# Optimization experiments

Measured on AMD Instinct MI355X. Metric: run time of the kernel, lower is better.

Reference implementation:

```python
import jax, jax.numpy as jnp
import numpy as np

T, N, E, F_IN, H1, H2, NUM_GRAPHS, K = 8, 10000, 320000, 32, 32, 16, 64, 5


def setup_inputs() -> dict:
    key = jax.random.key(0)
    ks = jax.random.split(key, 16)
    p = lambda k, shape: jax.random.normal(k, shape, jnp.float32) * 0.05
    return {
        "x": jax.random.normal(ks[0], (T, N, F_IN), jnp.float32),
        "edge_index": jax.random.randint(ks[1], (2, E), 0, N),
        "edge_attr": jax.random.uniform(ks[2], (E,), jnp.float32),
        "batch": jnp.sort(jax.random.randint(ks[3], (N,), 0, NUM_GRAPHS)),
        "Wx1": p(ks[4], (4, K, F_IN, H1)),
        "bx1": jnp.zeros((4, H1), jnp.float32),
        "Wh1": p(ks[5], (4, K, H1, H1)),
        "bh1": jnp.zeros((4, H1), jnp.float32),
        "wc1": p(ks[6], (3, H1)),
        "b1": jnp.zeros((4, H1), jnp.float32),
        "Wx2": p(ks[7], (4, K, H1, H2)),
        "bx2": jnp.zeros((4, H2), jnp.float32),
        "Wh2": p(ks[8], (4, K, H2, H2)),
        "bh2": jnp.zeros((4, H2), jnp.float32),
        "wc2": p(ks[9], (3, H2)),
        "b2": jnp.zeros((4, H2), jnp.float32),
        "lin_w": p(ks[10], (H2, 1)),
        "lin_b": jnp.zeros((1,), jnp.float32),
    }


def _forward(x, edge_index, edge_attr, batch,
             Wx1, bx1, Wh1, bh1, wc1, b1,
             Wx2, bx2, Wh2, bh2, wc2, b2, lin_w, lin_b):
    src, dst = edge_index[0], edge_index[1]
    n = x.shape[1]

    # ChebConv sym normalization with lambda_max=2: L_hat = L_sym - I = -D^{-1/2} A D^{-1/2}
    deg = jax.ops.segment_sum(edge_attr, src, num_segments=n)
    deg_safe = jnp.where(deg > 0, deg, 1.0)
    dis = jnp.where(deg > 0, jax.lax.rsqrt(deg_safe), 0.0)
    wnorm = dis[src] * edge_attr * dis[dst]  # [E]

    def Lhat(z):  # z: [N, C] -> L_hat @ z
        return -jax.ops.segment_sum(wnorm[:, None] * z[src], dst, num_segments=n)

    def cheb(z, W, b):  # W: [K, C_in, C_out], b: [C_out]
        out = z @ W[0]
        Tp, Tc = z, Lhat(z)  # T_0, T_1
        out = out + Tc @ W[1]
        for k in range(2, W.shape[0]):
            Tp, Tc = Tc, 2.0 * Lhat(Tc) - Tp
            out = out + Tc @ W[k]
        return out + b

    def cell(X, H, C, Wx, bx, Wh, bh, wc, bg):
        # gate order: 0=i, 1=f, 2=c, 3=o (GConvLSTM with peepholes)
        I = jax.nn.sigmoid(cheb(X, Wx[0], bx[0]) + cheb(H, Wh[0], bh[0]) + wc[0] * C + bg[0])
        Fg = jax.nn.sigmoid(cheb(X, Wx[1], bx[1]) + cheb(H, Wh[1], bh[1]) + wc[1] * C + bg[1])
        Ct = jnp.tanh(cheb(X, Wx[2], bx[2]) + cheb(H, Wh[2], bh[2]) + bg[2])
        Cn = Fg * C + I * Ct
        O = jax.nn.sigmoid(cheb(X, Wx[3], bx[3]) + cheb(H, Wh[3], bh[3]) + wc[2] * Cn + bg[3])
        return O * jnp.tanh(Cn), Cn

    @jax.checkpoint
    def step(carry, xt):
        h1, c1, h2, c2 = carry
        h1, c1 = cell(xt, h1, c1, Wx1, bx1, Wh1, bh1, wc1, b1)
        h2, c2 = cell(h1, h2, c2, Wx2, bx2, Wh2, bh2, wc2, b2)
        return (h1, c1, h2, c2), None

    z32 = jnp.zeros((n, Wh1.shape[-1]), x.dtype)
    z16 = jnp.zeros((n, Wh2.shape[-1]), x.dtype)
    (h1, c1, h2, c2), _ = jax.lax.scan(step, (z32, z32, z16, z16), x)

    # relu/dropout on h2 in the torch code is dead code (its result is unused in eval)
    u = jax.ops.segment_sum(h2, batch, num_segments=NUM_GRAPHS)  # global_add_pool
    return (u @ lin_w + lin_b).reshape(-1)


def reference(x, edge_index, edge_attr, batch,
              Wx1, bx1, Wh1, bh1, wc1, b1,
              Wx2, bx2, Wh2, bh2, wc2, b2, lin_w, lin_b):
    return _forward(x, edge_index, edge_attr, batch,
                    Wx1, bx1, Wh1, bh1, wc1, b1,
                    Wx2, bx2, Wh2, bh2, wc2, b2, lin_w, lin_b)
```

## Files before the change

### kernel.cpp

```cpp
#include <hip/hip_runtime.h>
#include <hip/hip_bf16.h>

#define TT 8
#define NN 10000
#define EE 320000
#define NG 64
#define SZS 400
#define SZH 384

typedef short v8s __attribute__((ext_vector_type(8)));
typedef _Float16 v8h __attribute__((ext_vector_type(8)));
typedef float v4f __attribute__((ext_vector_type(4)));

__device__ __forceinline__ float sigmf(float x){ return 1.f/(1.f+expf(-x)); }
__device__ __forceinline__ unsigned short f2h(float f){ _Float16 h=(_Float16)f; return __builtin_bit_cast(unsigned short,h); }
__device__ __forceinline__ float h2f(unsigned short s){ return (float)__builtin_bit_cast(_Float16,s); }
__device__ __forceinline__ unsigned pack2h(float x,float y){ return (unsigned)f2h(x) | ((unsigned)f2h(y)<<16); }
__device__ __forceinline__ size_t fragidx(int TK,int row,int c){
  int tile=row>>4, m=row&15, kt=c>>5, cc=c&31;
  return ((size_t)(tile*TK+kt)*64 + (cc>>3)*16 + m)*8 + (cc&7);
}

__global__ void k_deg(const int* __restrict__ src, const float* __restrict__ ea, float* __restrict__ deg){
  int e = blockIdx.x*256 + threadIdx.x;
  if(e<EE) atomicAdd(&deg[src[e]], ea[e]);
}

__global__ void k_dis(const float* __restrict__ deg, float* __restrict__ dis){
  int n = blockIdx.x*256+threadIdx.x;
  if(n<NN){ float d=deg[n]; dis[n] = d>0.f ? rsqrtf(d) : 0.f; }
}

__global__ void k_wnorm(const int* __restrict__ src, const int* __restrict__ dst, const float* __restrict__ ea,
                        const float* __restrict__ dis, float* __restrict__ wnorm, int* __restrict__ cnt){
  int e = blockIdx.x*256+threadIdx.x;
  if(e<EE){
    int s=src[e], d=dst[e];
    wnorm[e] = dis[s]*ea[e]*dis[d];
    atomicAdd(&cnt[d],1);
  }
}

__global__ __launch_bounds__(1024) void k_scan(const int* __restrict__ cnt, int* __restrict__ rowptr, int* __restrict__ wp){
  __shared__ int wsum[16];
  __shared__ int carrysh;
  int tid=threadIdx.x, lane=tid&63, wv=tid>>6;
  if(tid==0){ carrysh=0; rowptr[0]=0; }
  __syncthreads();
  for(int base=0;base<NN;base+=1024){
    int i=base+tid;
    int v=(i<NN)?cnt[i]:0;
    int s=v;
    #pragma unroll
    for(int d=1;d<64;d<<=1){ int t=__shfl_up(s,d,64); if(lane>=d) s+=t; }
    if(lane==63) wsum[wv]=s;
    __syncthreads();
    if(wv==0 && lane<16){
      int t=wsum[lane]; int ss=t;
      #pragma unroll
      for(int d=1;d<16;d<<=1){ int u=__shfl_up(ss,d,64); if(lane>=d) ss+=u; }
      wsum[lane]=ss-t;
    }
    __syncthreads();
    int total = carrysh + wsum[wv] + s;
    if(i<NN) rowptr[i+1]=total;
    __syncthreads();
    if(tid==1023) carrysh = total;
    __syncthreads();
  }
  for(int i=tid;i<NN;i+=1024) wp[i]=rowptr[i];
}

__global__ void k_scatter(const int* __restrict__ src, const int* __restrict__ dst, const float* __restrict__ wnorm,
                          int* __restrict__ wp, int2* __restrict__ pack){
  int e = blockIdx.x*256+threadIdx.x;
  if(e<EE){
    int d=dst[e];
    int pos = atomicAdd(&wp[d],1);
    pack[pos] = make_int2(src[e], __float_as_int(wnorm[e]));
  }
}

__device__ __forceinline__ float fetchW1(const float* Wx, const float* Wh, int kk, int col){
  int g=col>>5, j=col&31;
  if(kk<160){ int k=kk>>5, i=kk&31; return Wx[((g*5+k)*32+i)*32+j]; }
  int rr=kk-160; int k=rr>>5, i=rr&31; return Wh[((g*5+k)*32+i)*32+j];
}
__device__ __forceinline__ float fetchW2(const float* Wx, const float* Wh, int kk, int col){
  int g=col>>4, j=col&15;
  if(kk<160){ int k=kk>>5, i=kk&31; return Wx[((g*5+k)*32+i)*16+j]; }
  if(kk<240){ int rr=kk-160; int k=rr>>4, i=rr&15; return Wh[((g*5+k)*16+i)*16+j]; }
  return 0.f;
}

__global__ void k_wreorg(const float* __restrict__ Wx1,const float* __restrict__ bx1,
                         const float* __restrict__ Wh1,const float* __restrict__ bh1,const float* __restrict__ b1,
                         const float* __restrict__ Wx2,const float* __restrict__ bx2,
                         const float* __restrict__ Wh2,const float* __restrict__ bh2,const float* __restrict__ b2g,
                         short* __restrict__ Wpk1, short* __restrict__ Wpk2,
                         float* __restrict__ Bc1,float* __restrict__ Bc2){
  int idx = blockIdx.x*256+threadIdx.x;
  if(idx < 5120){
    int lane=idx&63, rest=idx>>6;
    int nt=rest&7, kt=rest>>3;
    int col = nt*16 + (lane&15);
    int g = lane>>4;
    #pragma unroll
    for(int j=0;j<8;j++){
      int kk = kt*32 + 8*g + j;
      Wpk1[(size_t)idx*8+j]=(short)f2h(fetchW1(Wx1,Wh1,kk,col));
    }
  } else if(idx < 7168){
    int t=idx-5120;
    int lane=t&63, rest=t>>6;
    int nt=rest&3, kt=rest>>2;
    int col = nt*16 + (lane&15);
    int g = lane>>4;
    #pragma unroll
    for(int j=0;j<8;j++){
      int kk = kt*32 + 8*g + j;
      Wpk2[(size_t)t*8+j]=(short)f2h(fetchW2(Wx2,Wh2,kk,col));
    }
  } else if(idx < 7296){
    int i=idx-7168; int g=i>>5,j=i&31;
    Bc1[i]=bx1[g*32+j]+bh1[g*32+j]+b1[g*32+j];
  } else if(idx < 7360){
    int i=idx-7296; int g=i>>4,j=i&15;
    Bc2[i]=bx2[g*16+j]+bh2[g*16+j]+b2g[g*16+j];
  }
}

__global__ void k_init1(const float* __restrict__ xt, float* __restrict__ ZS,
                        unsigned short* __restrict__ ZH, short* __restrict__ Zb1){
  int idx=blockIdx.x*256+threadIdx.x;
  if(idx<NN*8){
    int n=idx>>3, c4=idx&7;
    float4 v = ((const float4*)xt)[idx];
    *(float4*)&ZS[(size_t)n*SZS + 240 + c4*4] = v;
    unsigned p0=pack2h(v.x,v.y), p1=pack2h(v.z,v.w);
    *(unsigned*)&ZH[(size_t)n*SZH + 48 + c4*4]     = p0;
    *(unsigned*)&ZH[(size_t)n*SZH + 48 + c4*4 + 2] = p1;
    size_t fi = fragidx(5, n, c4*4);
    *(unsigned*)&Zb1[fi]   = p0;
    *(unsigned*)&Zb1[fi+2] = p1;
  }
}

template<int MODE>
__global__ __launch_bounds__(256) void k_spmm(const int* __restrict__ rowptr, const int2* __restrict__ pack,
    float* __restrict__ ZS, unsigned short* __restrict__ ZH,
    short* __restrict__ Zb1, short* __restrict__ Zb2, int k){
  int wlocal = __builtin_amdgcn_readfirstlane(threadIdx.x>>6);
  int wid = blockIdx.x*4 + wlocal;
  if(wid>=NN) return;
  int l = threadIdx.x&63;
  int ch; bool act;
  if(MODE==0){ ch=48+2*l; act=(l<16); }
  else if(MODE==1){
    if(l<16) ch=2*l; else if(l<24) ch=32+2*(l-16); else ch=48+2*(l-24);
    act=(l<40);
  } else {
    if(l<16) ch=2*l; else ch=32+2*(l-16);
    act=(l<24);
  }
  if(!act) ch=(MODE==2)?0:48;
  int cin_h = (k-1)*96 + ch;
  int base,width,cloc;
  if(ch<32){ base=0; width=32; cloc=ch; }
  else if(ch<48){ base=160; width=16; cloc=ch-32; }
  else { base=240; width=32; cloc=ch-48; }
  int cout = base + k*width + cloc;
  int cpp  = base + (k-2)*width + cloc;
  const unsigned short* __restrict__ Zc = ZH + cin_h;
  int e0=rowptr[wid], e1=rowptr[wid+1];
  float accx=0.f, accy=0.f;
  int e=e0;
  for(; e+16<=e1; e+=16){
    float w[16]; unsigned z[16];
    #pragma unroll
    for(int j=0;j<16;j++){
      int2 p=pack[e+j];
      w[j]=__int_as_float(p.y);
      z[j]=*(const unsigned*)&Zc[(unsigned)p.x*SZH];
    }
    #pragma unroll
    for(int j=0;j<16;j++){
      accx += h2f((unsigned short)(z[j]&0xffffu))*w[j];
      accy += h2f((unsigned short)(z[j]>>16))*w[j];
    }
  }
  for(; e+4<=e1; e+=4){
    float w[4]; unsigned z[4];
    #pragma unroll
    for(int j=0;j<4;j++){ int2 p=pack[e+j]; w[j]=__int_as_float(p.y); z[j]=*(const unsigned*)&Zc[(unsigned)p.x*SZH]; }
    #pragma unroll
    for(int j=0;j<4;j++){
      accx += h2f((unsigned short)(z[j]&0xffffu))*w[j];
      accy += h2f((unsigned short)(z[j]>>16))*w[j];
    }
  }
  for(; e<e1; ++e){
    int2 p=pack[e];
    unsigned zz=*(const unsigned*)&Zc[(unsigned)p.x*SZH];
    float ww=__int_as_float(p.y);
    accx += h2f((unsigned short)(zz&0xffffu))*ww;
    accy += h2f((unsigned short)(zz>>16))*ww;
  }
  if(act){
    float alpha=(k==1)?1.f:2.f;
    float vx = -alpha*accx, vy = -alpha*accy;
    if(k>=2){
      float2 pp=*(const float2*)&ZS[(unsigned)wid*SZS+cpp];
      vx -= pp.x; vy -= pp.y;
    }
    *(float2*)&ZS[(unsigned)wid*SZS+cout]=make_float2(vx,vy);
    unsigned hh = pack2h(vx,vy);
    if(k<=3) *(unsigned*)&ZH[(size_t)wid*SZH + k*96 + ch] = hh;
    if(ch<48) *(unsigned*)&Zb2[fragidx(8,wid,cout)] = hh;
    else      *(unsigned*)&Zb1[fragidx(5,wid,cout-240)] = hh;
  }
}

__device__ __forceinline__ void gemm1_dev(int tile,int lane,
        const short* __restrict__ Zb1, const short* __restrict__ Zb2,
        const v8s* __restrict__ H1T0r, v8s* __restrict__ H1T0w,
        const short* __restrict__ Wpk, const float* __restrict__ Bc, const float* __restrict__ wc1,
        float* __restrict__ c1, float* __restrict__ ZS, unsigned short* __restrict__ ZH,
        short* __restrict__ Zb1w, const float* __restrict__ xn){
  const v8s* A1=(const v8s*)Zb1 + (size_t)tile*320 + lane;
  const v8s* A2=(const v8s*)Zb2 + (size_t)tile*512 + lane;
  v8h afr[10];
  #pragma unroll
  for(int kt=0;kt<5;kt++) afr[kt]=__builtin_bit_cast(v8h, A1[kt*64]);
  afr[5]=__builtin_bit_cast(v8h, H1T0r[(size_t)tile*64+lane]);
  #pragma unroll
  for(int kt=1;kt<5;kt++) afr[5+kt]=__builtin_bit_cast(v8h, A2[kt*64]);
  const v8s* Wp=(const v8s*)Wpk;
  v4f acc[8];
  #pragma unroll
  for(int nt=0;nt<8;nt++) acc[nt]=(v4f){0.f,0.f,0.f,0.f};
  #pragma unroll
  for(int kt=0;kt<10;kt++){
    #pragma unroll
    for(int nt=0;nt<8;nt++){
      v8h b=__builtin_bit_cast(v8h, Wp[(kt*8+nt)*64+lane]);
      acc[nt]=__builtin_amdgcn_mfma_f32_16x16x32_f16(afr[kt],b,acc[nt],0,0,0);
    }
  }
  int row0=tile*16;
  int j0=lane&15;
  int r0=row0+(lane>>4)*4;
  #pragma unroll
  for(int reg=0;reg<4;reg++){
    int row=r0+reg;
    #pragma unroll
    for(int jj=0;jj<2;jj++){
      int j=jj*16+j0;
      float c=c1[row*32+j];
      float I =sigmf(acc[0+jj][reg]+Bc[j]      + wc1[j]*c);
      float Fg=sigmf(acc[2+jj][reg]+Bc[32+j]   + wc1[32+j]*c);
      float Ct=tanhf(acc[4+jj][reg]+Bc[64+j]);
      float Cn=Fg*c + I*Ct;
      float O =sigmf(acc[6+jj][reg]+Bc[96+j]   + wc1[64+j]*Cn);
      float h =O*tanhf(Cn);
      c1[row*32+j]=Cn;
      ZS[(size_t)row*SZS + j]=h;
      ZH[(size_t)row*SZH + j]=f2h(h);
      ((unsigned short*)H1T0w)[fragidx(1,row,j)]=f2h(h);
    }
    if(xn){
      float2 xv=*(const float2*)&xn[(size_t)row*32 + 2*j0];
      *(float2*)&ZS[(size_t)row*SZS + 240 + 2*j0]=xv;
      unsigned pr=pack2h(xv.x,xv.y);
      *(unsigned*)&ZH[(size_t)row*SZH + 48 + 2*j0]=pr;
      *(unsigned*)&Zb1w[fragidx(5,row,2*j0)]=pr;
    }
  }
}

__device__ __forceinline__ void gemm2_dev(int tile,int lane,
        const short* __restrict__ Zb2, const v8s* __restrict__ H1T0r,
        const short* __restrict__ Wpk, const float* __restrict__ Bc, const float* __restrict__ wc2,
        float* __restrict__ c2, float* __restrict__ ZS, unsigned short* __restrict__ ZH,
        short* __restrict__ Zb2w, float* __restrict__ u, const int* __restrict__ batch, int last){
  const v8s* Az=(const v8s*)Zb2 + (size_t)tile*512 + lane;
  v8h afr[8];
  afr[0]=__builtin_bit_cast(v8h, H1T0r[(size_t)tile*64+lane]);
  #pragma unroll
  for(int kt=1;kt<8;kt++) afr[kt]=__builtin_bit_cast(v8h, Az[kt*64]);
  const v8s* Wp=(const v8s*)Wpk;
  v4f acc[4];
  #pragma unroll
  for(int nt=0;nt<4;nt++) acc[nt]=(v4f){0.f,0.f,0.f,0.f};
  #pragma unroll
  for(int kt=0;kt<8;kt++){
    #pragma unroll
    for(int nt=0;nt<4;nt++){
      v8h b=__builtin_bit_cast(v8h, Wp[(kt*4+nt)*64+lane]);
      acc[nt]=__builtin_amdgcn_mfma_f32_16x16x32_f16(afr[kt],b,acc[nt],0,0,0);
    }
  }
  int row0=tile*16;
  int j=lane&15;
  int r0=row0+(lane>>4)*4;
  #pragma unroll
  for(int reg=0;reg<4;reg++){
    int row=r0+reg;
    float c=c2[row*16+j];
    float I =sigmf(acc[0][reg]+Bc[j]    +wc2[j]*c);
    float Fg=sigmf(acc[1][reg]+Bc[16+j] +wc2[16+j]*c);
    float Ct=tanhf(acc[2][reg]+Bc[32+j]);
    float Cn=Fg*c+I*Ct;
    float O =sigmf(acc[3][reg]+Bc[48+j] +wc2[32+j]*Cn);
    float h =O*tanhf(Cn);
    c2[row*16+j]=Cn;
    ZS[(size_t)row*SZS + 160 + j]=h;
    ZH[(size_t)row*SZH + 32 + j]=f2h(h);
    Zb2w[fragidx(8,row,160+j)]=(short)f2h(h);
    if(last) atomicAdd(&u[batch[row]*16+j], h);
  }
}

__global__ __launch_bounds__(256) void k_g1(const short* Zb1, const short* Zb2,
        const v8s* H1T0r, v8s* H1T0w, const short* Wpk1, const float* Bc1, const float* wc1,
        float* c1, float* ZS, unsigned short* ZH, short* Zb1w, const float* xn){
  int wv=threadIdx.x>>6, lane=threadIdx.x&63;
  int tile=blockIdx.x*4+wv;
  if(tile>=625) return;
  gemm1_dev(tile,lane,Zb1,Zb2,H1T0r,H1T0w,Wpk1,Bc1,wc1,c1,ZS,ZH,Zb1w,xn);
}

__global__ __launch_bounds__(256) void k_g2(const short* Zb2, const v8s* H1T0r,
        const short* Wpk2, const float* Bc2, const float* wc2,
        float* c2, float* ZS, unsigned short* ZH, short* Zb2w,
        float* u, const int* batch, int last){
  int wv=threadIdx.x>>6, lane=threadIdx.x&63;
  int tile=blockIdx.x*4+wv;
  if(tile>=625) return;
  gemm2_dev(tile,lane,Zb2,H1T0r,Wpk2,Bc2,wc2,c2,ZS,ZH,Zb2w,u,batch,last);
}

__global__ __launch_bounds__(256) void k_g12(const short* Zb1, const short* Zb2,
        const v8s* H1T0r, v8s* H1T0w,
        const short* Wpk1, const float* Bc1, const float* wc1, float* c1,
        const short* Wpk2, const float* Bc2, const float* wc2, float* c2,
        float* ZS, unsigned short* ZH, short* Zb1w, short* Zb2w,
        const float* xn, float* u, const int* batch){
  int wv=threadIdx.x>>6, lane=threadIdx.x&63;
  if(blockIdx.x<157){
    int tile=blockIdx.x*4+wv;
    if(tile>=625) return;
    gemm1_dev(tile,lane,Zb1,Zb2,H1T0r,H1T0w,Wpk1,Bc1,wc1,c1,ZS,ZH,Zb1w,xn);
  } else {
    int tile=(blockIdx.x-157)*4+wv;
    if(tile>=625) return;
    gemm2_dev(tile,lane,Zb2,H1T0r,Wpk2,Bc2,wc2,c2,ZS,ZH,Zb2w,u,batch,0);
  }
}

__global__ void k_final(const float* __restrict__ u, const float* __restrict__ lw, const float* __restrict__ lb,
                        float* __restrict__ out){
  int g=threadIdx.x;
  if(g<NG){
    float s=lb[0];
    #pragma unroll
    for(int j=0;j<16;j++) s += u[g*16+j]*lw[j];
    out[g]=s;
  }
}

extern "C" void kernel_launch(void* const* d_in, const int* in_sizes, int n_in,
                              void* d_out, int out_size, void* d_ws, size_t ws_size,
                              hipStream_t stream){
  const float* x   = (const float*)d_in[0];
  const int*   ei  = (const int*)d_in[1];
  const float* ea  = (const float*)d_in[2];
  const int*   bat = (const int*)d_in[3];
  const float* Wx1=(const float*)d_in[4];  const float* bx1=(const float*)d_in[5];
  const float* Wh1=(const float*)d_in[6];  const float* bh1=(const float*)d_in[7];
  const float* wc1=(const float*)d_in[8];  const float* b1 =(const float*)d_in[9];
  const float* Wx2=(const float*)d_in[10]; const float* bx2=(const float*)d_in[11];
  const float* Wh2=(const float*)d_in[12]; const float* bh2=(const float*)d_in[13];
  const float* wc2=(const float*)d_in[14]; const float* b2 =(const float*)d_in[15];
  const float* lw =(const float*)d_in[16]; const float* lb =(const float*)d_in[17];
  const int* src = ei; const int* dst = ei+EE;

  float* ws = (float*)d_ws;
  size_t off=0;
  auto alloc=[&](size_t n)->float*{ float* p=ws+off; off+=(n+15)&~(size_t)15; return p; };
  float* deg=alloc(NN);
  float* c1=alloc((size_t)NN*32);
  float* c2=alloc((size_t)NN*16);
  float* u =alloc(NG*16);
  int*   cnt=(int*)alloc(NN);
  float* ZS=alloc((size_t)NN*SZS);
  unsigned short* ZH=(unsigned short*)alloc((size_t)NN*SZH/2);
  short* Zb1=(short*)alloc(625*5*64*8/2);
  short* Zb2=(short*)alloc(625*8*64*8/2);
  short* H1T0a=(short*)alloc(625*64*8/2);
  short* H1T0b=(short*)alloc(625*64*8/2);
  size_t zeroEnd=off;
  float* dis=alloc(NN);
  float* wnorm=alloc(EE);
  int*   rowptr=(int*)alloc(NN+1);
  int*   wp=(int*)alloc(NN);
  int2*  pack=(int2*)alloc((size_t)EE*2);
  short* Wpk1=(short*)alloc(5120*4);
  short* Wpk2=(short*)alloc(2048*4);
  float* Bc1=alloc(128);     float* Bc2=alloc(64);
  (void)ws_size; (void)in_sizes; (void)n_in; (void)out_size;
  v8s* H1T0[2] = { (v8s*)H1T0a, (v8s*)H1T0b };

  hipMemsetAsync(d_ws, 0, zeroEnd*sizeof(float), stream);
  k_deg    <<<1250,256,0,stream>>>(src,ea,deg);
  k_dis    <<<40,256,0,stream>>>(deg,dis);
  k_wnorm  <<<1250,256,0,stream>>>(src,dst,ea,dis,wnorm,cnt);
  k_scan   <<<1,1024,0,stream>>>(cnt,rowptr,wp);
  k_scatter<<<1250,256,0,stream>>>(src,dst,wnorm,wp,pack);
  k_wreorg <<<29,256,0,stream>>>(Wx1,bx1,Wh1,bh1,b1,Wx2,bx2,Wh2,bh2,b2,Wpk1,Wpk2,Bc1,Bc2);

  k_init1<<<313,256,0,stream>>>(x, ZS, ZH, Zb1);
  for(int k=1;k<5;k++)
    k_spmm<0><<<2500,256,0,stream>>>(rowptr,pack,ZS,ZH,Zb1,Zb2,k);

  k_g1<<<157,256,0,stream>>>(Zb1,Zb2,H1T0[1],H1T0[0],Wpk1,Bc1,wc1,c1,ZS,ZH,Zb1, x+(size_t)NN*32);

  for(int t=0;t<TT-1;t++){
    for(int k=1;k<5;k++)
      k_spmm<1><<<2500,256,0,stream>>>(rowptr,pack,ZS,ZH,Zb1,Zb2,k);
    k_g12<<<314,256,0,stream>>>(Zb1,Zb2,H1T0[t&1],H1T0[(t+1)&1],
        Wpk1,Bc1,wc1,c1, Wpk2,Bc2,wc2,c2, ZS,ZH,Zb1,Zb2,
        (t+2<TT)? x+(size_t)(t+2)*NN*32 : nullptr, u,bat);
  }
  for(int k=1;k<5;k++)
    k_spmm<2><<<2500,256,0,stream>>>(rowptr,pack,ZS,ZH,Zb1,Zb2,k);
  k_g2<<<157,256,0,stream>>>(Zb2,H1T0[(TT-1)&1],Wpk2,Bc2,wc2,c2,ZS,ZH,Zb2,u,bat,1);

  k_final<<<1,64,0,stream>>>(u,lw,lb,(float*)d_out);
}
```

Measured before the change: 617.6 us.

## Drop fp32 ZS shadow buffer, fuse setup kernels, widen spmm blocks

Removes the fp32 ZS staging buffer entirely. The Chebyshev recurrence now reads the T_{k-2} term from the fp16 ZH buffer, and the fp32 stores in the gemm and init paths are gone. The deg, weight-reorg and init kernels are merged into a single setup launch, and spmm moves to 512-thread blocks with 8 rows per block. This cuts memory traffic and launch count, but the T_{k-2} subtraction now uses fp16-rounded values, which can add precision error.

New measurement: 583.4 us. 1.06x faster.

```diff
diff --git a/kernel.cpp b/kernel.cpp
--- a/kernel.cpp
+++ b/kernel.cpp
@@ -5,7 +5,6 @@
 #define NN 10000
 #define EE 320000
 #define NG 64
-#define SZS 400
 #define SZH 384
 
 typedef short v8s __attribute__((ext_vector_type(8)));
@@ -21,9 +20,66 @@
   return ((size_t)(tile*TK+kt)*64 + (cc>>3)*16 + m)*8 + (cc&7);
 }
 
-__global__ void k_deg(const int* __restrict__ src, const float* __restrict__ ea, float* __restrict__ deg){
-  int e = blockIdx.x*256 + threadIdx.x;
-  if(e<EE) atomicAdd(&deg[src[e]], ea[e]);
+__device__ __forceinline__ float fetchW1(const float* Wx, const float* Wh, int kk, int col){
+  int g=col>>5, j=col&31;
+  if(kk<160){ int k=kk>>5, i=kk&31; return Wx[((g*5+k)*32+i)*32+j]; }
+  int rr=kk-160; int k=rr>>5, i=rr&31; return Wh[((g*5+k)*32+i)*32+j];
+}
+__device__ __forceinline__ float fetchW2(const float* Wx, const float* Wh, int kk, int col){
+  int g=col>>4, j=col&15;
+  if(kk<160){ int k=kk>>5, i=kk&31; return Wx[((g*5+k)*32+i)*16+j]; }
+  if(kk<240){ int rr=kk-160; int k=rr>>4, i=rr&15; return Wh[((g*5+k)*16+i)*16+j]; }
+  return 0.f;
+}
+
+__global__ void k_setup0(const int* __restrict__ src, const float* __restrict__ ea, float* __restrict__ deg,
+                         const float* __restrict__ Wx1,const float* __restrict__ bx1,
+                         const float* __restrict__ Wh1,const float* __restrict__ bh1,const float* __restrict__ b1,
+                         const float* __restrict__ Wx2,const float* __restrict__ bx2,
+                         const float* __restrict__ Wh2,const float* __restrict__ bh2,const float* __restrict__ b2g,
+                         short* __restrict__ Wpk1, short* __restrict__ Wpk2,
+                         float* __restrict__ Bc1,float* __restrict__ Bc2,
+                         const float* __restrict__ x, unsigned short* __restrict__ ZH, short* __restrict__ Zb1){
+  int idx = blockIdx.x*256+threadIdx.x;
+  if(idx<EE) atomicAdd(&deg[src[idx]], ea[idx]);
+  if(idx < 5120){
+    int lane=idx&63, rest=idx>>6;
+    int nt=rest&7, kt=rest>>3;
+    int col = nt*16 + (lane&15);
+    int g = lane>>4;
+    #pragma unroll
+    for(int j=0;j<8;j++){
+      int kk = kt*32 + 8*g + j;
+      Wpk1[(size_t)idx*8+j]=(short)f2h(fetchW1(Wx1,Wh1,kk,col));
+    }
+  } else if(idx < 7168){
+    int t=idx-5120;
+    int lane=t&63, rest=t>>6;
+    int nt=rest&3, kt=rest>>2;
+    int col = nt*16 + (lane&15);
+    int g = lane>>4;
+    #pragma unroll
+    for(int j=0;j<8;j++){
+      int kk = kt*32 + 8*g + j;
+      Wpk2[(size_t)t*8+j]=(short)f2h(fetchW2(Wx2,Wh2,kk,col));
+    }
+  } else if(idx < 7296){
+    int i=idx-7168; int g=i>>5,j=i&31;
+    Bc1[i]=bx1[g*32+j]+bh1[g*32+j]+b1[g*32+j];
+  } else if(idx < 7360){
+    int i=idx-7296; int g=i>>4,j=i&15;
+    Bc2[i]=bx2[g*16+j]+bh2[g*16+j]+b2g[g*16+j];
+  }
+  if(idx<NN*8){
+    int n=idx>>3, c4=idx&7;
+    float4 v = ((const float4*)x)[idx];
+    unsigned p0=pack2h(v.x,v.y), p1=pack2h(v.z,v.w);
+    *(unsigned*)&ZH[(size_t)n*SZH + 48 + c4*4]     = p0;
+    *(unsigned*)&ZH[(size_t)n*SZH + 48 + c4*4 + 2] = p1;
+    size_t fi = fragidx(5, n, c4*4);
+    *(unsigned*)&Zb1[fi]   = p0;
+    *(unsigned*)&Zb1[fi+2] = p1;
+  }
 }
 
 __global__ void k_dis(const float* __restrict__ deg, float* __restrict__ dis){
@@ -81,77 +137,12 @@
   }
 }
 
-__device__ __forceinline__ float fetchW1(const float* Wx, const float* Wh, int kk, int col){
-  int g=col>>5, j=col&31;
-  if(kk<160){ int k=kk>>5, i=kk&31; return Wx[((g*5+k)*32+i)*32+j]; }
-  int rr=kk-160; int k=rr>>5, i=rr&31; return Wh[((g*5+k)*32+i)*32+j];
-}
-__device__ __forceinline__ float fetchW2(const float* Wx, const float* Wh, int kk, int col){
-  int g=col>>4, j=col&15;
-  if(kk<160){ int k=kk>>5, i=kk&31; return Wx[((g*5+k)*32+i)*16+j]; }
-  if(kk<240){ int rr=kk-160; int k=rr>>4, i=rr&15; return Wh[((g*5+k)*16+i)*16+j]; }
-  return 0.f;
-}
-
-__global__ void k_wreorg(const float* __restrict__ Wx1,const float* __restrict__ bx1,
-                         const float* __restrict__ Wh1,const float* __restrict__ bh1,const float* __restrict__ b1,
-                         const float* __restrict__ Wx2,const float* __restrict__ bx2,
-                         const float* __restrict__ Wh2,const float* __restrict__ bh2,const float* __restrict__ b2g,
-                         short* __restrict__ Wpk1, short* __restrict__ Wpk2,
-                         float* __restrict__ Bc1,float* __restrict__ Bc2){
-  int idx = blockIdx.x*256+threadIdx.x;
-  if(idx < 5120){
-    int lane=idx&63, rest=idx>>6;
-    int nt=rest&7, kt=rest>>3;
-    int col = nt*16 + (lane&15);
-    int g = lane>>4;
-    #pragma unroll
-    for(int j=0;j<8;j++){
-      int kk = kt*32 + 8*g + j;
-      Wpk1[(size_t)idx*8+j]=(short)f2h(fetchW1(Wx1,Wh1,kk,col));
-    }
-  } else if(idx < 7168){
-    int t=idx-5120;
-    int lane=t&63, rest=t>>6;
-    int nt=rest&3, kt=rest>>2;
-    int col = nt*16 + (lane&15);
-    int g = lane>>4;
-    #pragma unroll
-    for(int j=0;j<8;j++){
-      int kk = kt*32 + 8*g + j;
-      Wpk2[(size_t)t*8+j]=(short)f2h(fetchW2(Wx2,Wh2,kk,col));
-    }
-  } else if(idx < 7296){
-    int i=idx-7168; int g=i>>5,j=i&31;
-    Bc1[i]=bx1[g*32+j]+bh1[g*32+j]+b1[g*32+j];
-  } else if(idx < 7360){
-    int i=idx-7296; int g=i>>4,j=i&15;
-    Bc2[i]=bx2[g*16+j]+bh2[g*16+j]+b2g[g*16+j];
-  }
-}
-
-__global__ void k_init1(const float* __restrict__ xt, float* __restrict__ ZS,
-                        unsigned short* __restrict__ ZH, short* __restrict__ Zb1){
-  int idx=blockIdx.x*256+threadIdx.x;
-  if(idx<NN*8){
-    int n=idx>>3, c4=idx&7;
-    float4 v = ((const float4*)xt)[idx];
-    *(float4*)&ZS[(size_t)n*SZS + 240 + c4*4] = v;
-    unsigned p0=pack2h(v.x,v.y), p1=pack2h(v.z,v.w);
-    *(unsigned*)&ZH[(size_t)n*SZH + 48 + c4*4]     = p0;
-    *(unsigned*)&ZH[(size_t)n*SZH + 48 + c4*4 + 2] = p1;
-    size_t fi = fragidx(5, n, c4*4);
-    *(unsigned*)&Zb1[fi]   = p0;
-    *(unsigned*)&Zb1[fi+2] = p1;
-  }
-}
-
 template<int MODE>
-__global__ __launch_bounds__(256) void k_spmm(const int* __restrict__ rowptr, const int2* __restrict__ pack,
-    float* __restrict__ ZS, unsigned short* __restrict__ ZH,
+__global__ __launch_bounds__(512) void k_spmm(const int* __restrict__ rowptr, const int2* __restrict__ pack,
+    unsigned short* __restrict__ ZH,
     short* __restrict__ Zb1, short* __restrict__ Zb2, int k){
   int wlocal = __builtin_amdgcn_readfirstlane(threadIdx.x>>6);
-  int wid = blockIdx.x*4 + wlocal;
+  int wid = blockIdx.x*8 + wlocal;
   if(wid>=NN) return;
   int l = threadIdx.x&63;
   int ch; bool act;
@@ -170,7 +161,6 @@
   else if(ch<48){ base=160; width=16; cloc=ch-32; }
   else { base=240; width=32; cloc=ch-48; }
   int cout = base + k*width + cloc;
-  int cpp  = base + (k-2)*width + cloc;
   const unsigned short* __restrict__ Zc = ZH + cin_h;
   int e0=rowptr[wid], e1=rowptr[wid+1];
   float accx=0.f, accy=0.f;
@@ -210,10 +200,10 @@
     float alpha=(k==1)?1.f:2.f;
     float vx = -alpha*accx, vy = -alpha*accy;
     if(k>=2){
-      float2 pp=*(const float2*)&ZS[(unsigned)wid*SZS+cpp];
-      vx -= pp.x; vy -= pp.y;
-    }
-    *(float2*)&ZS[(unsigned)wid*SZS+cout]=make_float2(vx,vy);
+      unsigned pp=*(const unsigned*)&ZH[(size_t)wid*SZH+(k-2)*96+ch];
+      vx -= h2f((unsigned short)(pp&0xffffu));
+      vy -= h2f((unsigned short)(pp>>16));
+    }
     unsigned hh = pack2h(vx,vy);
     if(k<=3) *(unsigned*)&ZH[(size_t)wid*SZH + k*96 + ch] = hh;
     if(ch<48) *(unsigned*)&Zb2[fragidx(8,wid,cout)] = hh;
@@ -225,7 +215,7 @@
         const short* __restrict__ Zb1, const short* __restrict__ Zb2,
         const v8s* __restrict__ H1T0r, v8s* __restrict__ H1T0w,
         const short* __restrict__ Wpk, const float* __restrict__ Bc, const float* __restrict__ wc1,
-        float* __restrict__ c1, float* __restrict__ ZS, unsigned short* __restrict__ ZH,
+        float* __restrict__ c1, unsigned short* __restrict__ ZH,
         short* __restrict__ Zb1w, const float* __restrict__ xn){
   const v8s* A1=(const v8s*)Zb1 + (size_t)tile*320 + lane;
   const v8s* A2=(const v8s*)Zb2 + (size_t)tile*512 + lane;
@@ -264,13 +254,11 @@
       float O =sigmf(acc[6+jj][reg]+Bc[96+j]   + wc1[64+j]*Cn);
       float h =O*tanhf(Cn);
       c1[row*32+j]=Cn;
-      ZS[(size_t)row*SZS + j]=h;
       ZH[(size_t)row*SZH + j]=f2h(h);
       ((unsigned short*)H1T0w)[fragidx(1,row,j)]=f2h(h);
     }
     if(xn){
       float2 xv=*(const float2*)&xn[(size_t)row*32 + 2*j0];
-      *(float2*)&ZS[(size_t)row*SZS + 240 + 2*j0]=xv;
       unsigned pr=pack2h(xv.x,xv.y);
       *(unsigned*)&ZH[(size_t)row*SZH + 48 + 2*j0]=pr;
       *(unsigned*)&Zb1w[fragidx(5,row,2*j0)]=pr;
@@ -281,7 +269,7 @@
 __device__ __forceinline__ void gemm2_dev(int tile,int lane,
         const short* __restrict__ Zb2, const v8s* __restrict__ H1T0r,
         const short* __restrict__ Wpk, const float* __restrict__ Bc, const float* __restrict__ wc2,
-        float* __restrict__ c2, float* __restrict__ ZS, unsigned short* __restrict__ ZH,
+        float* __restrict__ c2, unsigned short* __restrict__ ZH,
         short* __restrict__ Zb2w, float* __restrict__ u, const int* __restrict__ batch, int last){
   const v8s* Az=(const v8s*)Zb2 + (size_t)tile*512 + lane;
   v8h afr[8];
@@ -314,7 +302,6 @@
     float O =sigmf(acc[3][reg]+Bc[48+j] +wc2[32+j]*Cn);
     float h =O*tanhf(Cn);
     c2[row*16+j]=Cn;
-    ZS[(size_t)row*SZS + 160 + j]=h;
     ZH[(size_t)row*SZH + 32 + j]=f2h(h);
     Zb2w[fragidx(8,row,160+j)]=(short)f2h(h);
     if(last) atomicAdd(&u[batch[row]*16+j], h);
@@ -323,38 +310,38 @@
 
 __global__ __launch_bounds__(256) void k_g1(const short* Zb1, const short* Zb2,
         const v8s* H1T0r, v8s* H1T0w, const short* Wpk1, const float* Bc1, const float* wc1,
-        float* c1, float* ZS, unsigned short* ZH, short* Zb1w, const float* xn){
+        float* c1, unsigned short* ZH, short* Zb1w, const float* xn){
   int wv=threadIdx.x>>6, lane=threadIdx.x&63;
   int tile=blockIdx.x*4+wv;
   if(tile>=625) return;
-  gemm1_dev(tile,lane,Zb1,Zb2,H1T0r,H1T0w,Wpk1,Bc1,wc1,c1,ZS,ZH,Zb1w,xn);
+  gemm1_dev(tile,lane,Zb1,Zb2,H1T0r,H1T0w,Wpk1,Bc1,wc1,c1,ZH,Zb1w,xn);
 }
 
 __global__ __launch_bounds__(256) void k_g2(const short* Zb2, const v8s* H1T0r,
         const short* Wpk2, const float* Bc2, const float* wc2,
-        float* c2, float* ZS, unsigned short* ZH, short* Zb2w,
+        float* c2, unsigned short* ZH, short* Zb2w,
         float* u, const int* batch, int last){
   int wv=threadIdx.x>>6, lane=threadIdx.x&63;
   int tile=blockIdx.x*4+wv;
   if(tile>=625) return;
-  gemm2_dev(tile,lane,Zb2,H1T0r,Wpk2,Bc2,wc2,c2,ZS,ZH,Zb2w,u,batch,last);
+  gemm2_dev(tile,lane,Zb2,H1T0r,Wpk2,Bc2,wc2,c2,ZH,Zb2w,u,batch,last);
 }
 
 __global__ __launch_bounds__(256) void k_g12(const short* Zb1, const short* Zb2,
         const v8s* H1T0r, v8s* H1T0w,
         const short* Wpk1, const float* Bc1, const float* wc1, float* c1,
         const short* Wpk2, const float* Bc2, const float* wc2, float* c2,
-        float* ZS, unsigned short* ZH, short* Zb1w, short* Zb2w,
+        unsigned short* ZH, short* Zb1w, short* Zb2w,
         const float* xn, float* u, const int* batch){
   int wv=threadIdx.x>>6, lane=threadIdx.x&63;
   if(blockIdx.x<157){
     int tile=blockIdx.x*4+wv;
     if(tile>=625) return;
-    gemm1_dev(tile,lane,Zb1,Zb2,H1T0r,H1T0w,Wpk1,Bc1,wc1,c1,ZS,ZH,Zb1w,xn);
+    gemm1_dev(tile,lane,Zb1,Zb2,H1T0r,H1T0w,Wpk1,Bc1,wc1,c1,ZH,Zb1w,xn);
   } else {
     int tile=(blockIdx.x-157)*4+wv;
     if(tile>=625) return;
-    gemm2_dev(tile,lane,Zb2,H1T0r,Wpk2,Bc2,wc2,c2,ZS,ZH,Zb2w,u,batch,0);
+    gemm2_dev(tile,lane,Zb2,H1T0r,Wpk2,Bc2,wc2,c2,ZH,Zb2w,u,batch,0);
   }
 }
 
@@ -393,7 +380,6 @@
   float* c2=alloc((size_t)NN*16);
   float* u =alloc(NG*16);
   int*   cnt=(int*)alloc(NN);
-  float* ZS=alloc((size_t)NN*SZS);
   unsigned short* ZH=(unsigned short*)alloc((size_t)NN*SZH/2);
   short* Zb1=(short*)alloc(625*5*64*8/2);
   short* Zb2=(short*)alloc(625*8*64*8/2);
@@ -412,29 +398,28 @@
   v8s* H1T0[2] = { (v8s*)H1T0a, (v8s*)H1T0b };
 
   hipMemsetAsync(d_ws, 0, zeroEnd*sizeof(float), stream);
-  k_deg    <<<1250,256,0,stream>>>(src,ea,deg);
+  k_setup0 <<<1250,256,0,stream>>>(src,ea,deg,
+      Wx1,bx1,Wh1,bh1,b1,Wx2,bx2,Wh2,bh2,b2,Wpk1,Wpk2,Bc1,Bc2, x,ZH,Zb1);
   k_dis    <<<40,256,0,stream>>>(deg,dis);
   k_wnorm  <<<1250,256,0,stream>>>(src,dst,ea,dis,wnorm,cnt);
   k_scan   <<<1,1024,0,stream>>>(cnt,rowptr,wp);
   k_scatter<<<1250,256,0,stream>>>(src,dst,wnorm,wp,pack);
-  k_wreorg <<<29,256,0,stream>>>(Wx1,bx1,Wh1,bh1,b1,Wx2,bx2,Wh2,bh2,b2,Wpk1,Wpk2,Bc1,Bc2);
-
-  k_init1<<<313,256,0,stream>>>(x, ZS, ZH, Zb1);
+
   for(int k=1;k<5;k++)
-    k_spmm<0><<<2500,256,0,stream>>>(rowptr,pack,ZS,ZH,Zb1,Zb2,k);
-
-  k_g1<<<157,256,0,stream>>>(Zb1,Zb2,H1T0[1],H1T0[0],Wpk1,Bc1,wc1,c1,ZS,ZH,Zb1, x+(size_t)NN*32);
+    k_spmm<0><<<1250,512,0,stream>>>(rowptr,pack,ZH,Zb1,Zb2,k);
+
+  k_g1<<<157,256,0,stream>>>(Zb1,Zb2,H1T0[1],H1T0[0],Wpk1,Bc1,wc1,c1,ZH,Zb1, x+(size_t)NN*32);
 
   for(int t=0;t<TT-1;t++){
     for(int k=1;k<5;k++)
-      k_spmm<1><<<2500,256,0,stream>>>(rowptr,pack,ZS,ZH,Zb1,Zb2,k);
+      k_spmm<1><<<1250,512,0,stream>>>(rowptr,pack,ZH,Zb1,Zb2,k);
     k_g12<<<314,256,0,stream>>>(Zb1,Zb2,H1T0[t&1],H1T0[(t+1)&1],
-        Wpk1,Bc1,wc1,c1, Wpk2,Bc2,wc2,c2, ZS,ZH,Zb1,Zb2,
+        Wpk1,Bc1,wc1,c1, Wpk2,Bc2,wc2,c2, ZH,Zb1,Zb2,
         (t+2<TT)? x+(size_t)(t+2)*NN*32 : nullptr, u,bat);
   }
   for(int k=1;k<5;k++)
-    k_spmm<2><<<2500,256,0,stream>>>(rowptr,pack,ZS,ZH,Zb1,Zb2,k);
-  k_g2<<<157,256,0,stream>>>(Zb2,H1T0[(TT-1)&1],Wpk2,Bc2,wc2,c2,ZS,ZH,Zb2,u,bat,1);
+    k_spmm<2><<<1250,512,0,stream>>>(rowptr,pack,ZH,Zb1,Zb2,k);
+  k_g2<<<157,256,0,stream>>>(Zb2,H1T0[(TT-1)&1],Wpk2,Bc2,wc2,c2,ZH,Zb2,u,bat,1);
 
   k_final<<<1,64,0,stream>>>(u,lw,lb,(float*)d_out);
 }
```
